# Optimization experiments

Hardware: AMD Instinct MI355X
Metric: run time of the kernel (lower is better)

## Reference

```python
import jax, jax.numpy as jnp
import numpy as np

B, C, N, H = 4, 256, 1024, 8
D = C // H
EPS = 1e-5

def setup_inputs() -> dict:
    key = jax.random.key(0)
    ks = jax.random.split(key, 10)
    s = lambda k, shape: (jax.random.normal(k, shape, jnp.float32) * 0.02)
    return dict(
        node_embeds=jax.random.normal(ks[0], (B, C, N), jnp.float32),
        edge_embeds=jax.random.normal(ks[1], (B, N, N), jnp.float32),
        da_prior=jax.random.normal(ks[2], (B, N, C), jnp.float32),
        gamma=jnp.ones((C,), jnp.float32),
        beta=jnp.zeros((C,), jnp.float32),
        w_qkv=s(ks[3], (C, 3 * C)),            # Linear(node_dim, 3*node_dim), no bias
        w_proj=s(ks[4], (C, C)),
        b_proj=jnp.zeros((C,), jnp.float32),
        w_expand=s(ks[5], (H,)),               # Conv2d(1,H,1) weight (per-head scalar)
        b_expand=jnp.zeros((H,), jnp.float32),
        w_reduce=s(ks[6], (H,)),               # Conv2d(H,1,1) weight
        b_reduce=jnp.zeros((1,), jnp.float32),
        w_fc=s(ks[7], (1, C)),                 # Linear(edge_dim=1, node_dim)
        b_fc=jnp.zeros((C,), jnp.float32),
    )

def reference(node_embeds, edge_embeds, da_prior, gamma, beta, w_qkv,
              w_proj, b_proj, w_expand, b_expand, w_reduce, b_reduce, w_fc, b_fc):
    x = jnp.swapaxes(node_embeds, 1, 2)                       # [B,N,C]
    # einsum 'bnn,bnc->bnc': diagonal of edge matrix scales each node
    diag = jnp.diagonal(edge_embeds, axis1=1, axis2=2)        # [B,N]
    attned = diag[:, :, None] * x                             # [B,N,C]
    # einsum 'bnc,bca->bnc' with prior permuted [B,C,A]: multiply by sum over A
    prior_sum = da_prior.sum(axis=1)                          # [B,C]
    x = attned * prior_sum[:, None, :] + x                    # residual add
    # LayerNorm over channel dim
    mu = x.mean(-1, keepdims=True)
    var = x.var(-1, keepdims=True)
    ln = (x - mu) * jax.lax.rsqrt(var + EPS) * gamma + beta
    qkv = (ln @ w_qkv).reshape(B, N, 3, H, D)
    q = jnp.transpose(qkv[:, :, 0], (0, 2, 1, 3))             # [B,H,N,D]
    k = jnp.transpose(qkv[:, :, 1], (0, 2, 1, 3))
    v = jnp.transpose(qkv[:, :, 2], (0, 2, 1, 3))
    scale = D ** -0.5
    attn = jnp.einsum('bhnd,bhmd->bhnm', q, k) * scale        # [B,H,N,N]
    bias = edge_embeds[:, None] * w_expand[None, :, None, None] + b_expand[None, :, None, None]
    attn = attn + bias                                        # pre-softmax scores = residual
    a = jax.nn.softmax(attn, axis=-1)
    node = jnp.einsum('bhnm,bhmd->bnhd', a, v).reshape(B, N, C)
    # reduce conv over heads on (softmax + residual)
    edge = jnp.einsum('bhnm,h->bnm', a + attn, w_reduce) + b_reduce[0]  # [B,N,N]
    w = jax.nn.softmax(edge, axis=-1)
    wsum = (w * edge).sum(-1)                                 # [B,N]
    node = node + wsum[:, :, None] @ w_fc + b_fc              # fc: [B,N,1]@[1,C]
    node = node @ w_proj + b_proj
    return jnp.swapaxes(node, 1, 2), edge                     # ([B,C,N], [B,N,N])
```

## Files before the change

### kernel.cpp

```cpp
#include <hip/hip_runtime.h>
#include <math.h>

#define Bn 4
#define Cn 256
#define Nn 1024
#define Hn 8
#define Dn 32
#define BHND (Bn * Hn * Nn * Dn)
#define BHN  (Bn * Hn * Nn)

typedef short bf16x8 __attribute__((ext_vector_type(8)));
typedef float f32x4 __attribute__((ext_vector_type(4)));

__device__ inline unsigned f2bf_rn_bits(float x) {
  union { float f; unsigned u; } v; v.f = x;
  return (v.u + 0x7FFFu + ((v.u >> 16) & 1u)) >> 16;
}
__device__ inline float bfbits2f(unsigned b) {
  union { unsigned u; float f; } v; v.u = b << 16; return v.f;
}
__device__ inline void split_bf(float x, unsigned& hi, unsigned& lo) {
  hi = f2bf_rn_bits(x);
  lo = f2bf_rn_bits(x - bfbits2f(hi));
}
__device__ inline unsigned split_bf_trunc_pack(float x) {
  union { float f; unsigned u; } v; v.f = x;
  unsigned hi = v.u >> 16;
  union { unsigned u; float f; } hv; hv.u = hi << 16;
  union { float f; unsigned u; } r; r.f = x - hv.f;
  return hi | (r.u & 0xffff0000u);
}
__device__ inline void unpack_u32x8(const uint4& a, const uint4& b, bf16x8& hi, bf16x8& lo) {
  int4 h4, l4;
  h4.x = (int)((a.x & 0xffffu) | (a.y << 16));  l4.x = (int)((a.x >> 16) | (a.y & 0xffff0000u));
  h4.y = (int)((a.z & 0xffffu) | (a.w << 16));  l4.y = (int)((a.z >> 16) | (a.w & 0xffff0000u));
  h4.z = (int)((b.x & 0xffffu) | (b.y << 16));  l4.z = (int)((b.x >> 16) | (b.y & 0xffff0000u));
  h4.w = (int)((b.z & 0xffffu) | (b.w << 16));  l4.w = (int)((b.z >> 16) | (b.w & 0xffff0000u));
  hi = *(bf16x8*)&h4; lo = *(bf16x8*)&l4;
}

__global__ __launch_bounds__(256) void k_prior_part(const float* __restrict__ dap,
                                                    float* __restrict__ pp) {
  int bi = blockIdx.x;
  int b = bi >> 5, ch = bi & 31;
  int c = threadIdx.x;
  float s = 0.f;
  int n0 = ch * 32;
  for (int n = n0; n < n0 + 32; ++n) s += dap[(size_t)(b * Nn + n) * Cn + c];
  pp[(size_t)(b * 32 + ch) * Cn + c] = s;
}

__global__ __launch_bounds__(256) void k_prior_red(const float* __restrict__ pp,
                                                   float* __restrict__ prior) {
  int i = blockIdx.x * 256 + threadIdx.x;
  int b = i >> 8, c = i & 255;
  float s = 0.f;
  for (int ch = 0; ch < 32; ++ch) s += pp[(size_t)(b * 32 + ch) * Cn + c];
  prior[i] = s;
}

__global__ __launch_bounds__(256) void k_transpose(const float* __restrict__ ne,
                                                   float* __restrict__ xw) {
  __shared__ float tile[32][33];
  int bi = blockIdx.x;
  int b = bi >> 8, rem = bi & 255;
  int c0 = (rem >> 5) << 5;
  int n0 = (rem & 31) << 5;
  int tx = threadIdx.x & 31, ty = threadIdx.x >> 5;
#pragma unroll
  for (int i = 0; i < 4; ++i) {
    int c = c0 + ty + i * 8;
    tile[ty + i * 8][tx] = ne[(size_t)(b * Cn + c) * Nn + n0 + tx];
  }
  __syncthreads();
#pragma unroll
  for (int i = 0; i < 4; ++i) {
    int n = n0 + ty + i * 8;
    xw[(size_t)(b * Nn + n) * Cn + c0 + tx] = tile[tx][ty + i * 8];
  }
}

__global__ __launch_bounds__(256) void k_split_wt(const float* __restrict__ w,
                                                  short* __restrict__ wt_h,
                                                  short* __restrict__ wt_l) {
  __shared__ float tile[32][33];
  int bi = blockIdx.x;
  int j0 = (bi >> 3) << 5;
  int k0 = (bi & 7) << 5;
  int tx = threadIdx.x & 31, ty = threadIdx.x >> 5;
#pragma unroll
  for (int i = 0; i < 4; ++i)
    tile[ty + i * 8][tx] = w[(size_t)(k0 + ty + i * 8) * 768 + j0 + tx];
  __syncthreads();
#pragma unroll
  for (int i = 0; i < 4; ++i) {
    float v = tile[tx][ty + i * 8];
    unsigned hb, lb; split_bf(v, hb, lb);
    wt_h[(size_t)(j0 + ty + i * 8) * 256 + k0 + tx] = (short)hb;
    wt_l[(size_t)(j0 + ty + i * 8) * 256 + k0 + tx] = (short)lb;
  }
}

__global__ __launch_bounds__(256) void k_prep_ln(const float* __restrict__ xw,
                                                 const float* __restrict__ eg,
                                                 const float* __restrict__ prior,
                                                 const float* __restrict__ gamma,
                                                 const float* __restrict__ beta,
                                                 short* __restrict__ ln_h,
                                                 short* __restrict__ ln_l) {
  int bn = blockIdx.x;
  int b = bn >> 10, n = bn & 1023;
  int c = threadIdx.x;
  float x = xw[(size_t)bn * Cn + c];
  float dg = eg[(size_t)(b * Nn + n) * Nn + n];
  float x2 = x * (1.f + dg * prior[b * Cn + c]);
  float s = x2, qq = x2 * x2;
#pragma unroll
  for (int off = 32; off >= 1; off >>= 1) {
    s += __shfl_xor(s, off);
    qq += __shfl_xor(qq, off);
  }
  __shared__ float ss[4], sq[4];
  if ((c & 63) == 0) { ss[c >> 6] = s; sq[c >> 6] = qq; }
  __syncthreads();
  s = ss[0] + ss[1] + ss[2] + ss[3];
  qq = sq[0] + sq[1] + sq[2] + sq[3];
  float mu = s * (1.f / 256.f);
  float var = qq * (1.f / 256.f) - mu * mu;
  float r = rsqrtf(var + 1e-5f);
  float v = (x2 - mu) * r * gamma[c] + beta[c];
  unsigned hb, lb; split_bf(v, hb, lb);
  ln_h[(size_t)bn * Cn + c] = (short)hb;
  ln_l[(size_t)bn * Cn + c] = (short)lb;
}

__global__ __launch_bounds__(256) void k_qkv_mfma(
    const short* __restrict__ ln_h, const short* __restrict__ ln_l,
    const short* __restrict__ wt_h, const short* __restrict__ wt_l,
    short* __restrict__ q_hi, short* __restrict__ q_lo,
    short* __restrict__ k_hi, short* __restrict__ k_lo,
    short* __restrict__ vt_hi, short* __restrict__ vt_lo) {
  __shared__ float ct[64][65];
  int m0 = blockIdx.x * 64;
  int j0 = blockIdx.y * 64;
  int t = threadIdx.x, wid = t >> 6, l = t & 63;
  int lr = l & 15, lq = l >> 4;
  f32x4 acc[4] = {};
  const short* ah_p = ln_h + (size_t)(m0 + wid * 16 + lr) * 256 + lq * 8;
  const short* al_p = ln_l + (size_t)(m0 + wid * 16 + lr) * 256 + lq * 8;
  const short* bh_p = wt_h + (size_t)(j0 + lr) * 256 + lq * 8;
  const short* bl_p = wt_l + (size_t)(j0 + lr) * 256 + lq * 8;
#pragma unroll 2
  for (int k0 = 0; k0 < 256; k0 += 32) {
    bf16x8 ah = *(const bf16x8*)&ah_p[k0];
    bf16x8 al = *(const bf16x8*)&al_p[k0];
#pragma unroll
    for (int js = 0; js < 4; ++js) {
      bf16x8 bh = *(const bf16x8*)&bh_p[js * 16 * 256 + k0];
      bf16x8 bl = *(const bf16x8*)&bl_p[js * 16 * 256 + k0];
      acc[js] = __builtin_amdgcn_mfma_f32_16x16x32_bf16(al, bh, acc[js], 0, 0, 0);
      acc[js] = __builtin_amdgcn_mfma_f32_16x16x32_bf16(ah, bl, acc[js], 0, 0, 0);
      acc[js] = __builtin_amdgcn_mfma_f32_16x16x32_bf16(ah, bh, acc[js], 0, 0, 0);
    }
  }
#pragma unroll
  for (int js = 0; js < 4; ++js)
#pragma unroll
    for (int reg = 0; reg < 4; ++reg)
      ct[wid * 16 + lq * 4 + reg][js * 16 + lr] = acc[js][reg];
  __syncthreads();
  int b = m0 >> 10, n0 = m0 & 1023;
  int three = j0 >> 8;
  const float scale = 0.17677669529663687f;
  if (three == 2) {
    int jl = t >> 2;
    int n4 = (t & 3) * 16;
    int rem = (j0 & 255) + jl;
    int h = rem >> 5, d = rem & 31;
    short hs[16], ls[16];
#pragma unroll
    for (int u = 0; u < 16; ++u) {
      unsigned hb, lb;
      split_bf(ct[n4 + u][jl], hb, lb);
      hs[u] = (short)hb; ls[u] = (short)lb;
    }
    size_t ob = ((size_t)(b * Hn + h) * Dn + d) * Nn + n0 + n4;
    *(uint4*)&vt_hi[ob] = *(uint4*)&hs[0];
    *(uint4*)&vt_hi[ob + 8] = *(uint4*)&hs[8];
    *(uint4*)&vt_lo[ob] = *(uint4*)&ls[0];
    *(uint4*)&vt_lo[ob + 8] = *(uint4*)&ls[8];
  } else {
    int m_l = t & 63, half = t >> 6;
    int rem = (j0 & 255) + half * 16;
    int h = rem >> 5, ddb = rem & 31;
    int n = n0 + m_l;
    float sc = (three == 0) ? 1.0f : scale;
    short* dh = three ? k_hi : q_hi;
    short* dl = three ? k_lo : q_lo;
    short hs[16], ls[16];
#pragma unroll
    for (int u = 0; u < 16; ++u) {
      unsigned hb, lb;
      split_bf(ct[m_l][half * 16 + u] * sc, hb, lb);
      hs[u] = (short)hb; ls[u] = (short)lb;
    }
    size_t base = ((size_t)((b * Hn + h) * Nn + n)) * Dn + ddb;
    *(uint4*)&dh[base] = *(uint4*)&hs[0];
    *(uint4*)&dh[base + 8] = *(uint4*)&hs[8];
    *(uint4*)&dl[base] = *(uint4*)&ls[0];
    *(uint4*)&dl[base + 8] = *(uint4*)&ls[8];
  }
}

__global__ __launch_bounds__(256, 4) void k_attn_core(
    const short* __restrict__ q_hi, const short* __restrict__ q_lo,
    const short* __restrict__ k_hi, const short* __restrict__ k_lo,
    const short* __restrict__ vt_hi, const short* __restrict__ vt_lo,
    const float* __restrict__ eg,
    const float* __restrict__ w_expand, const float* __restrict__ b_expand,
    float* __restrict__ o_part, float* __restrict__ l_part) {
  __shared__ short kh[64 * 40];
  __shared__ short kl[64 * 40];
  __shared__ short vth[32 * 72];
  __shared__ short vtl[32 * 72];
  __shared__ unsigned pbuf[4][16 * 68];

  int blk = blockIdx.x;
  int mh = blk & 1;
  int nt = (blk >> 1) & 15;
  int h = (blk >> 5) & 7;
  int b = blk >> 8;
  int n0 = nt * 64;
  int t = threadIdx.x, wid = t >> 6, l = t & 63;
  int lr = l & 15, lq = l >> 4;

  const float we = w_expand[h], be = b_expand[h];
  size_t bhb = (size_t)(b * Hn + h) * Nn * Dn;
  const short* khg = k_hi + bhb;
  const short* klg = k_lo + bhb;
  const short* vhg = vt_hi + bhb;
  const short* vlg = vt_lo + bhb;

  bf16x8 qhi, qlo;
  {
    size_t qoff = bhb + (size_t)(n0 + wid * 16 + lr) * Dn + lq * 8;
    qhi = *(const bf16x8*)&q_hi[qoff];
    qlo = *(const bf16x8*)&q_lo[qoff];
  }

  f32x4 O0 = {0.f, 0.f, 0.f, 0.f}, O1 = {0.f, 0.f, 0.f, 0.f};
  float rowsum[4] = {0.f, 0.f, 0.f, 0.f};
  int nrow = n0 + wid * 16 + lq * 4;

  for (int ms = 0; ms < 8; ++ms) {
    int m0 = mh * 512 + ms * 64;
    float eb[4][4];
#pragma unroll
    for (int reg = 0; reg < 4; ++reg) {
      const float* ep = &eg[(size_t)(b * Nn + nrow + reg) * Nn + m0 + lr];
#pragma unroll
      for (int msub = 0; msub < 4; ++msub) eb[msub][reg] = ep[msub * 16];
    }
    __syncthreads();
    {
      int row = t >> 2, c = (t & 3) * 8;
      *(uint4*)&kh[row * 40 + c] = *(const uint4*)&khg[(size_t)(m0 + row) * Dn + c];
      *(uint4*)&kl[row * 40 + c] = *(const uint4*)&klg[(size_t)(m0 + row) * Dn + c];
      int d = t >> 3, cm = (t & 7) * 8;
      *(uint4*)&vth[d * 72 + cm] = *(const uint4*)&vhg[(size_t)d * Nn + m0 + cm];
      *(uint4*)&vtl[d * 72 + cm] = *(const uint4*)&vlg[(size_t)d * Nn + m0 + cm];
    }
    __syncthreads();

#pragma unroll
    for (int msub = 0; msub < 4; ++msub) {
      int mrow = msub * 16 + lr;
      bf16x8 bh8 = *(bf16x8*)&kh[mrow * 40 + lq * 8];
      bf16x8 bl8 = *(bf16x8*)&kl[mrow * 40 + lq * 8];
      f32x4 sacc = {0.f, 0.f, 0.f, 0.f};
      sacc = __builtin_amdgcn_mfma_f32_16x16x32_bf16(qlo, bh8, sacc, 0, 0, 0);
      sacc = __builtin_amdgcn_mfma_f32_16x16x32_bf16(qhi, bl8, sacc, 0, 0, 0);
      sacc = __builtin_amdgcn_mfma_f32_16x16x32_bf16(qhi, bh8, sacc, 0, 0, 0);
#pragma unroll
      for (int reg = 0; reg < 4; ++reg) {
        float s = sacc[reg] + eb[msub][reg] * we + be;
        float e = __expf(s);
        rowsum[reg] += e;
        pbuf[wid][(lq * 4 + reg) * 68 + msub * 16 + lr] = split_bf_trunc_pack(e);
      }
    }

#pragma unroll
    for (int mw = 0; mw < 2; ++mw) {
      uint4 pa = *(uint4*)&pbuf[wid][lr * 68 + mw * 32 + lq * 8];
      uint4 pb = *(uint4*)&pbuf[wid][lr * 68 + mw * 32 + lq * 8 + 4];
      bf16x8 ahi, alo;
      unpack_u32x8(pa, pb, ahi, alo);
      {
        bf16x8 vh8 = *(bf16x8*)&vth[lr * 72 + mw * 32 + lq * 8];
        bf16x8 vl8 = *(bf16x8*)&vtl[lr * 72 + mw * 32 + lq * 8];
        O0 = __builtin_amdgcn_mfma_f32_16x16x32_bf16(alo, vh8, O0, 0, 0, 0);
        O0 = __builtin_amdgcn_mfma_f32_16x16x32_bf16(ahi, vl8, O0, 0, 0, 0);
        O0 = __builtin_amdgcn_mfma_f32_16x16x32_bf16(ahi, vh8, O0, 0, 0, 0);
      }
      {
        bf16x8 vh8 = *(bf16x8*)&vth[(16 + lr) * 72 + mw * 32 + lq * 8];
        bf16x8 vl8 = *(bf16x8*)&vtl[(16 + lr) * 72 + mw * 32 + lq * 8];
        O1 = __builtin_amdgcn_mfma_f32_16x16x32_bf16(alo, vh8, O1, 0, 0, 0);
        O1 = __builtin_amdgcn_mfma_f32_16x16x32_bf16(ahi, vl8, O1, 0, 0, 0);
        O1 = __builtin_amdgcn_mfma_f32_16x16x32_bf16(ahi, vh8, O1, 0, 0, 0);
      }
    }
  }

#pragma unroll
  for (int reg = 0; reg < 4; ++reg) {
#pragma unroll
    for (int off = 1; off < 16; off <<= 1)
      rowsum[reg] += __shfl_xor(rowsum[reg], off);
  }
  size_t pbase = (size_t)mh * BHND + bhb;
#pragma unroll
  for (int reg = 0; reg < 4; ++reg) {
    int n = nrow + reg;
    o_part[pbase + (size_t)n * Dn + lr] = O0[reg];
    o_part[pbase + (size_t)n * Dn + 16 + lr] = O1[reg];
    if (lr == 0)
      l_part[(size_t)mh * BHN + (size_t)(b * Hn + h) * Nn + n] = rowsum[reg];
  }
}

__global__ __launch_bounds__(256, 4) void k_edge_mfma(
    const short* __restrict__ q_hi, const short* __restrict__ q_lo,
    const short* __restrict__ k_hi, const short* __restrict__ k_lo,
    const float* __restrict__ eg, const float* __restrict__ l_part,
    const float* __restrict__ w_expand, const float* __restrict__ b_expand,
    const float* __restrict__ w_reduce, const float* __restrict__ b_reduce,
    float* __restrict__ edge_out, float* __restrict__ pl_part,
    float* __restrict__ pwe_part) {
  __shared__ short kh[64 * 40];
  __shared__ short kl[64 * 40];
  int blk = blockIdx.x;
  int mt = blk & 15;
  int nt = (blk >> 4) & 15;
  int b = blk >> 8;
  int n0 = nt * 64, m0 = mt * 64;
  int t = threadIdx.x, wid = t >> 6, l = t & 63;
  int lr = l & 15, lq = l >> 4;
  const float br = b_reduce[0];
  int nrow = n0 + wid * 16 + lq * 4;

  float eacc[4][4], ebias[4][4];
#pragma unroll
  for (int reg = 0; reg < 4; ++reg) {
    const float* ep = &eg[(size_t)(b * Nn + nrow + reg) * Nn + m0 + lr];
#pragma unroll
    for (int msub = 0; msub < 4; ++msub) {
      ebias[msub][reg] = ep[msub * 16];
      eacc[msub][reg] = br;
    }
  }

  for (int h = 0; h < Hn; ++h) {
    size_t bhb = (size_t)(b * Hn + h) * Nn * Dn;
    float we = w_expand[h], be = b_expand[h], wr = w_reduce[h];
    bf16x8 qhi, qlo;
    {
      size_t qoff = bhb + (size_t)(n0 + wid * 16 + lr) * Dn + lq * 8;
      qhi = *(const bf16x8*)&q_hi[qoff];
      qlo = *(const bf16x8*)&q_lo[qoff];
    }
    float invl[4];
#pragma unroll
    for (int reg = 0; reg < 4; ++reg) {
      size_t idx = (size_t)(b * Hn + h) * Nn + nrow + reg;
      invl[reg] = 1.0f / (l_part[idx] + l_part[BHN + idx]);
    }

    __syncthreads();
    {
      int row = t >> 2, c = (t & 3) * 8;
      *(uint4*)&kh[row * 40 + c] = *(const uint4*)&k_hi[bhb + (size_t)(m0 + row) * Dn + c];
      *(uint4*)&kl[row * 40 + c] = *(const uint4*)&k_lo[bhb + (size_t)(m0 + row) * Dn + c];
    }
    __syncthreads();
#pragma unroll
    for (int msub = 0; msub < 4; ++msub) {
      int mrow = msub * 16 + lr;
      bf16x8 bh8 = *(bf16x8*)&kh[mrow * 40 + lq * 8];
      bf16x8 bl8 = *(bf16x8*)&kl[mrow * 40 + lq * 8];
      f32x4 sacc = {0.f, 0.f, 0.f, 0.f};
      sacc = __builtin_amdgcn_mfma_f32_16x16x32_bf16(qlo, bh8, sacc, 0, 0, 0);
      sacc = __builtin_amdgcn_mfma_f32_16x16x32_bf16(qhi, bl8, sacc, 0, 0, 0);
      sacc = __builtin_amdgcn_mfma_f32_16x16x32_bf16(qhi, bh8, sacc, 0, 0, 0);
#pragma unroll
      for (int reg = 0; reg < 4; ++reg) {
        float s = sacc[reg] + ebias[msub][reg] * we + be;
        float p = __expf(s) * invl[reg];
        eacc[msub][reg] += wr * (p + s);
      }
    }
  }
#pragma unroll
  for (int msub = 0; msub < 4; ++msub)
#pragma unroll
    for (int reg = 0; reg < 4; ++reg)
      edge_out[(size_t)(b * Nn + nrow + reg) * Nn + m0 + msub * 16 + lr] = eacc[msub][reg];

  float pl[4] = {0.f, 0.f, 0.f, 0.f}, pw[4] = {0.f, 0.f, 0.f, 0.f};
#pragma unroll
  for (int msub = 0; msub < 4; ++msub)
#pragma unroll
    for (int reg = 0; reg < 4; ++reg) {
      float e = eacc[msub][reg];
      float x = __expf(e);
      pl[reg] += x;
      pw[reg] += x * e;
    }
#pragma unroll
  for (int reg = 0; reg < 4; ++reg) {
#pragma unroll
    for (int off = 1; off < 16; off <<= 1) {
      pl[reg] += __shfl_xor(pl[reg], off);
      pw[reg] += __shfl_xor(pw[reg], off);
    }
    if (lr == 0) {
      int idx = mt * (Bn * Nn) + b * Nn + nrow + reg;
      pl_part[idx] = pl[reg];
      pwe_part[idx] = pw[reg];
    }
  }
}

__global__ __launch_bounds__(256) void k_edge_red(const float* __restrict__ pl,
                                                  const float* __restrict__ pwe,
                                                  float* __restrict__ wsum) {
  int i = blockIdx.x * 256 + threadIdx.x;
  float L = 0.f, Wv = 0.f;
  for (int mt = 0; mt < 16; ++mt) {
    L += pl[mt * (Bn * Nn) + i];
    Wv += pwe[mt * (Bn * Nn) + i];
  }
  wsum[i] = Wv / L;
}

__global__ __launch_bounds__(256) void k_proj_gemm(const float* __restrict__ o_part,
                                                   const float* __restrict__ l_part,
                                                   const float* __restrict__ wsum,
                                                   const float* __restrict__ wfc,
                                                   const float* __restrict__ bfc,
                                                   const float* __restrict__ wproj,
                                                   const float* __restrict__ bproj,
                                                   float* __restrict__ out) {
  __shared__ __align__(16) float at[16][68];
  __shared__ __align__(16) float bt[16][68];
  __shared__ float ct[64][65];
  int m0 = blockIdx.x * 64;
  int j0 = blockIdx.y * 64;
  int t = threadIdx.x;
  int tx = t & 15, ty = t >> 4;
  float4 acc[4] = {};
  for (int k0 = 0; k0 < 256; k0 += 16) {
    {
      int row = t >> 2, k4 = (t & 3) << 2;
      int m = m0 + row;
      int bb = m >> 10, n = m & 1023;
      int c = k0 + k4;
      int h = c >> 5, dd = c & 31;
      float wsm = wsum[m];
      size_t ob = ((size_t)(bb * Hn + h) * Nn + n) * Dn + dd;
      float4 oa = *(const float4*)&o_part[ob];
      float4 oc = *(const float4*)&o_part[BHND + ob];
      size_t sidx = (size_t)(bb * Hn + h) * Nn + n;
      float inv = 1.0f / (l_part[sidx] + l_part[BHN + sidx]);
      float4 a;
      a.x = (oa.x + oc.x) * inv + wsm * wfc[c + 0] + bfc[c + 0];
      a.y = (oa.y + oc.y) * inv + wsm * wfc[c + 1] + bfc[c + 1];
      a.z = (oa.z + oc.z) * inv + wsm * wfc[c + 2] + bfc[c + 2];
      a.w = (oa.w + oc.w) * inv + wsm * wfc[c + 3] + bfc[c + 3];
      at[k4 + 0][row] = a.x; at[k4 + 1][row] = a.y;
      at[k4 + 2][row] = a.z; at[k4 + 3][row] = a.w;
      int rb = t >> 4, jb = (t & 15) << 2;
      *(float4*)&bt[rb][jb] = *(const float4*)&wproj[(size_t)(k0 + rb) * 256 + j0 + jb];
    }
    __syncthreads();
#pragma unroll
    for (int kk = 0; kk < 16; ++kk) {
      float4 a4 = *(float4*)&at[kk][ty << 2];
      float4 b4 = *(float4*)&bt[kk][tx << 2];
      acc[0].x += a4.x * b4.x; acc[0].y += a4.x * b4.y; acc[0].z += a4.x * b4.z; acc[0].w += a4.x * b4.w;
      acc[1].x += a4.y * b4.x; acc[1].y += a4.y * b4.y; acc[1].z += a4.y * b4.z; acc[1].w += a4.y * b4.w;
      acc[2].x += a4.z * b4.x; acc[2].y += a4.z * b4.y; acc[2].z += a4.z * b4.z; acc[2].w += a4.z * b4.w;
      acc[3].x += a4.w * b4.x; acc[3].y += a4.w * b4.y; acc[3].z += a4.w * b4.z; acc[3].w += a4.w * b4.w;
    }
    __syncthreads();
  }
#pragma unroll
  for (int i = 0; i < 4; ++i) {
    ct[(ty << 2) + i][(tx << 2) + 0] = acc[i].x + bproj[j0 + (tx << 2) + 0];
    ct[(ty << 2) + i][(tx << 2) + 1] = acc[i].y + bproj[j0 + (tx << 2) + 1];
    ct[(ty << 2) + i][(tx << 2) + 2] = acc[i].z + bproj[j0 + (tx << 2) + 2];
    ct[(ty << 2) + i][(tx << 2) + 3] = acc[i].w + bproj[j0 + (tx << 2) + 3];
  }
  __syncthreads();
  int b = m0 >> 10, n0 = m0 & 1023;
  int n4 = t & 15, c0i = t >> 4;
#pragma unroll
  for (int u = 0; u < 4; ++u) {
    int ci = c0i + u * 16;
    float4 val = { ct[(n4 << 2) + 0][ci], ct[(n4 << 2) + 1][ci],
                   ct[(n4 << 2) + 2][ci], ct[(n4 << 2) + 3][ci] };
    *(float4*)&out[(size_t)(b * Cn + j0 + ci) * Nn + n0 + (n4 << 2)] = val;
  }
}

extern "C" void kernel_launch(void* const* d_in, const int* in_sizes, int n_in,
                              void* d_out, int out_size, void* d_ws, size_t ws_size,
                              hipStream_t stream) {
  (void)in_sizes; (void)n_in; (void)out_size; (void)ws_size;
  const float* node_embeds = (const float*)d_in[0];
  const float* edge_embeds = (const float*)d_in[1];
  const float* da_prior    = (const float*)d_in[2];
  const float* gamma       = (const float*)d_in[3];
  const float* beta        = (const float*)d_in[4];
  const float* w_qkv       = (const float*)d_in[5];
  const float* w_proj      = (const float*)d_in[6];
  const float* b_proj      = (const float*)d_in[7];
  const float* w_expand    = (const float*)d_in[8];
  const float* b_expand    = (const float*)d_in[9];
  const float* w_reduce    = (const float*)d_in[10];
  const float* b_reduce    = (const float*)d_in[11];
  const float* w_fc        = (const float*)d_in[12];
  const float* b_fc        = (const float*)d_in[13];
  float* out_node = (float*)d_out;
  float* out_edge = out_node + (size_t)Bn * Cn * Nn;

  const size_t M = 1048576;
  float* W = (float*)d_ws;
  float* ws_x   = W;
  short* ln_hi  = (short*)(W + M);
  short* ln_lo  = ln_hi + M;
  float* o_part = W;
  short* vt_hi  = (short*)(W + 2 * M);
  short* vt_lo  = vt_hi + M;
  short* q_hi   = (short*)(W + 3 * M);
  short* q_lo   = q_hi + M;
  short* k_hi   = q_hi + 2 * M;
  short* k_lo   = q_hi + 3 * M;
  float* ws_pp    = W + 5 * M;
  float* ws_prior = ws_pp + Bn * 32 * Cn;
  float* ws_wsum  = ws_prior + Bn * Cn;
  float* l_part   = ws_wsum + Bn * Nn;
  float* pl_part  = l_part + 2 * BHN;
  float* pwe_part = pl_part + 16 * Bn * Nn;
  short* wt_hi    = (short*)(pwe_part + 16 * Bn * Nn);
  short* wt_lo    = wt_hi + 768 * 256;

  k_split_wt<<<dim3(192), dim3(256), 0, stream>>>(w_qkv, wt_hi, wt_lo);
  k_prior_part<<<dim3(Bn * 32), dim3(256), 0, stream>>>(da_prior, ws_pp);
  k_prior_red<<<dim3(Bn), dim3(256), 0, stream>>>(ws_pp, ws_prior);
  k_transpose<<<dim3(Bn * 256), dim3(256), 0, stream>>>(node_embeds, ws_x);
  k_prep_ln<<<dim3(Bn * Nn), dim3(256), 0, stream>>>(ws_x, edge_embeds, ws_prior,
                                                     gamma, beta, ln_hi, ln_lo);
  k_qkv_mfma<<<dim3(64, 12), dim3(256), 0, stream>>>(ln_hi, ln_lo, wt_hi, wt_lo,
                                                     q_hi, q_lo, k_hi, k_lo,
                                                     vt_hi, vt_lo);
  k_attn_core<<<dim3(Bn * Hn * 16 * 2), dim3(256), 0, stream>>>(
      q_hi, q_lo, k_hi, k_lo, vt_hi, vt_lo, edge_embeds, w_expand, b_expand,
      o_part, l_part);
  k_edge_mfma<<<dim3(Bn * 16 * 16), dim3(256), 0, stream>>>(
      q_hi, q_lo, k_hi, k_lo, edge_embeds, l_part, w_expand, b_expand,
      w_reduce, b_reduce, out_edge, pl_part, pwe_part);
  k_edge_red<<<dim3(16), dim3(256), 0, stream>>>(pl_part, pwe_part, ws_wsum);
  k_proj_gemm<<<dim3(64, 4), dim3(256), 0, stream>>>(o_part, l_part, ws_wsum,
                                                     w_fc, b_fc, w_proj, b_proj,
                                                     out_node);
}
```

Before: 206.2 us.

## Fuse small preprocessing and reduction kernels to cut launch count

Merges the prior partial sum and the weight split/transpose into one kernel. The transpose kernel is dropped: the LayerNorm prep now reads node_embeds directly with a strided column access and finishes the prior reduction inline. The edge-softmax reduction moves into the projection GEMM prologue. This cuts four launches and several workspace round trips. In exchange, the LayerNorm kernel's global reads become uncoalesced and the projection blocks repeat a small reduction.

```diff
diff --git a/kernel.cpp b/kernel.cpp
--- a/kernel.cpp
+++ b/kernel.cpp
@@ -39,71 +39,42 @@
   hi = *(bf16x8*)&h4; lo = *(bf16x8*)&l4;
 }
 
-__global__ __launch_bounds__(256) void k_prior_part(const float* __restrict__ dap,
-                                                    float* __restrict__ pp) {
-  int bi = blockIdx.x;
-  int b = bi >> 5, ch = bi & 31;
-  int c = threadIdx.x;
-  float s = 0.f;
-  int n0 = ch * 32;
-  for (int n = n0; n < n0 + 32; ++n) s += dap[(size_t)(b * Nn + n) * Cn + c];
-  pp[(size_t)(b * 32 + ch) * Cn + c] = s;
-}
-
-__global__ __launch_bounds__(256) void k_prior_red(const float* __restrict__ pp,
-                                                   float* __restrict__ prior) {
-  int i = blockIdx.x * 256 + threadIdx.x;
-  int b = i >> 8, c = i & 255;
-  float s = 0.f;
-  for (int ch = 0; ch < 32; ++ch) s += pp[(size_t)(b * 32 + ch) * Cn + c];
-  prior[i] = s;
-}
-
-__global__ __launch_bounds__(256) void k_transpose(const float* __restrict__ ne,
-                                                   float* __restrict__ xw) {
+__global__ __launch_bounds__(256) void k_pre(const float* __restrict__ w,
+                                             const float* __restrict__ dap,
+                                             short* __restrict__ wt_h,
+                                             short* __restrict__ wt_l,
+                                             float* __restrict__ pp) {
   __shared__ float tile[32][33];
   int bi = blockIdx.x;
-  int b = bi >> 8, rem = bi & 255;
-  int c0 = (rem >> 5) << 5;
-  int n0 = (rem & 31) << 5;
-  int tx = threadIdx.x & 31, ty = threadIdx.x >> 5;
-#pragma unroll
-  for (int i = 0; i < 4; ++i) {
-    int c = c0 + ty + i * 8;
-    tile[ty + i * 8][tx] = ne[(size_t)(b * Cn + c) * Nn + n0 + tx];
-  }
-  __syncthreads();
-#pragma unroll
-  for (int i = 0; i < 4; ++i) {
-    int n = n0 + ty + i * 8;
-    xw[(size_t)(b * Nn + n) * Cn + c0 + tx] = tile[tx][ty + i * 8];
-  }
-}
-
-__global__ __launch_bounds__(256) void k_split_wt(const float* __restrict__ w,
-                                                  short* __restrict__ wt_h,
-                                                  short* __restrict__ wt_l) {
-  __shared__ float tile[32][33];
-  int bi = blockIdx.x;
-  int j0 = (bi >> 3) << 5;
-  int k0 = (bi & 7) << 5;
-  int tx = threadIdx.x & 31, ty = threadIdx.x >> 5;
-#pragma unroll
-  for (int i = 0; i < 4; ++i)
-    tile[ty + i * 8][tx] = w[(size_t)(k0 + ty + i * 8) * 768 + j0 + tx];
-  __syncthreads();
-#pragma unroll
-  for (int i = 0; i < 4; ++i) {
-    float v = tile[tx][ty + i * 8];
-    unsigned hb, lb; split_bf(v, hb, lb);
-    wt_h[(size_t)(j0 + ty + i * 8) * 256 + k0 + tx] = (short)hb;
-    wt_l[(size_t)(j0 + ty + i * 8) * 256 + k0 + tx] = (short)lb;
-  }
-}
-
-__global__ __launch_bounds__(256) void k_prep_ln(const float* __restrict__ xw,
+  if (bi < 32) {
+    int b = bi >> 3, ch = bi & 7;
+    int c = threadIdx.x;
+    float s = 0.f;
+    int n0 = ch * 128;
+    for (int n = n0; n < n0 + 128; ++n) s += dap[(size_t)(b * Nn + n) * Cn + c];
+    pp[(size_t)bi * Cn + c] = s;
+  } else {
+    int wi = bi - 32;
+    int j0 = (wi >> 3) << 5;
+    int k0 = (wi & 7) << 5;
+    int tx = threadIdx.x & 31, ty = threadIdx.x >> 5;
+#pragma unroll
+    for (int i = 0; i < 4; ++i)
+      tile[ty + i * 8][tx] = w[(size_t)(k0 + ty + i * 8) * 768 + j0 + tx];
+    __syncthreads();
+#pragma unroll
+    for (int i = 0; i < 4; ++i) {
+      float v = tile[tx][ty + i * 8];
+      unsigned hb, lb; split_bf(v, hb, lb);
+      wt_h[(size_t)(j0 + ty + i * 8) * 256 + k0 + tx] = (short)hb;
+      wt_l[(size_t)(j0 + ty + i * 8) * 256 + k0 + tx] = (short)lb;
+    }
+  }
+}
+
+__global__ __launch_bounds__(256) void k_prep_ln(const float* __restrict__ ne,
                                                  const float* __restrict__ eg,
-                                                 const float* __restrict__ prior,
+                                                 const float* __restrict__ pp,
                                                  const float* __restrict__ gamma,
                                                  const float* __restrict__ beta,
                                                  short* __restrict__ ln_h,
@@ -111,9 +82,12 @@
   int bn = blockIdx.x;
   int b = bn >> 10, n = bn & 1023;
   int c = threadIdx.x;
-  float x = xw[(size_t)bn * Cn + c];
+  float x = ne[(size_t)(b * Cn + c) * Nn + n];
+  float pr = 0.f;
+#pragma unroll
+  for (int ch = 0; ch < 8; ++ch) pr += pp[(size_t)(b * 8 + ch) * Cn + c];
   float dg = eg[(size_t)(b * Nn + n) * Nn + n];
-  float x2 = x * (1.f + dg * prior[b * Cn + c]);
+  float x2 = x * (1.f + dg * pr);
   float s = x2, qq = x2 * x2;
 #pragma unroll
   for (int off = 32; off >= 1; off >>= 1) {
@@ -432,21 +406,10 @@
   }
 }
 
-__global__ __launch_bounds__(256) void k_edge_red(const float* __restrict__ pl,
-                                                  const float* __restrict__ pwe,
-                                                  float* __restrict__ wsum) {
-  int i = blockIdx.x * 256 + threadIdx.x;
-  float L = 0.f, Wv = 0.f;
-  for (int mt = 0; mt < 16; ++mt) {
-    L += pl[mt * (Bn * Nn) + i];
-    Wv += pwe[mt * (Bn * Nn) + i];
-  }
-  wsum[i] = Wv / L;
-}
-
 __global__ __launch_bounds__(256) void k_proj_gemm(const float* __restrict__ o_part,
                                                    const float* __restrict__ l_part,
-                                                   const float* __restrict__ wsum,
+                                                   const float* __restrict__ pl,
+                                                   const float* __restrict__ pwe,
                                                    const float* __restrict__ wfc,
                                                    const float* __restrict__ bfc,
                                                    const float* __restrict__ wproj,
@@ -455,10 +418,22 @@
   __shared__ __align__(16) float at[16][68];
   __shared__ __align__(16) float bt[16][68];
   __shared__ float ct[64][65];
+  __shared__ float wsm_s[64];
   int m0 = blockIdx.x * 64;
   int j0 = blockIdx.y * 64;
   int t = threadIdx.x;
   int tx = t & 15, ty = t >> 4;
+  if (t < 64) {
+    int m = m0 + t;
+    float L = 0.f, Wv = 0.f;
+#pragma unroll
+    for (int mt = 0; mt < 16; ++mt) {
+      L += pl[mt * (Bn * Nn) + m];
+      Wv += pwe[mt * (Bn * Nn) + m];
+    }
+    wsm_s[t] = Wv / L;
+  }
+  __syncthreads();
   float4 acc[4] = {};
   for (int k0 = 0; k0 < 256; k0 += 16) {
     {
@@ -467,7 +442,7 @@
       int bb = m >> 10, n = m & 1023;
       int c = k0 + k4;
       int h = c >> 5, dd = c & 31;
-      float wsm = wsum[m];
+      float wsm = wsm_s[row];
       size_t ob = ((size_t)(bb * Hn + h) * Nn + n) * Dn + dd;
       float4 oa = *(const float4*)&o_part[ob];
       float4 oc = *(const float4*)&o_part[BHND + ob];
@@ -537,7 +512,6 @@
 
   const size_t M = 1048576;
   float* W = (float*)d_ws;
-  float* ws_x   = W;
   short* ln_hi  = (short*)(W + M);
   short* ln_lo  = ln_hi + M;
   float* o_part = W;
@@ -548,19 +522,14 @@
   short* k_hi   = q_hi + 2 * M;
   short* k_lo   = q_hi + 3 * M;
   float* ws_pp    = W + 5 * M;
-  float* ws_prior = ws_pp + Bn * 32 * Cn;
-  float* ws_wsum  = ws_prior + Bn * Cn;
-  float* l_part   = ws_wsum + Bn * Nn;
+  float* l_part   = ws_pp + Bn * 8 * Cn;
   float* pl_part  = l_part + 2 * BHN;
   float* pwe_part = pl_part + 16 * Bn * Nn;
   short* wt_hi    = (short*)(pwe_part + 16 * Bn * Nn);
   short* wt_lo    = wt_hi + 768 * 256;
 
-  k_split_wt<<<dim3(192), dim3(256), 0, stream>>>(w_qkv, wt_hi, wt_lo);
-  k_prior_part<<<dim3(Bn * 32), dim3(256), 0, stream>>>(da_prior, ws_pp);
-  k_prior_red<<<dim3(Bn), dim3(256), 0, stream>>>(ws_pp, ws_prior);
-  k_transpose<<<dim3(Bn * 256), dim3(256), 0, stream>>>(node_embeds, ws_x);
-  k_prep_ln<<<dim3(Bn * Nn), dim3(256), 0, stream>>>(ws_x, edge_embeds, ws_prior,
+  k_pre<<<dim3(224), dim3(256), 0, stream>>>(w_qkv, da_prior, wt_hi, wt_lo, ws_pp);
+  k_prep_ln<<<dim3(Bn * Nn), dim3(256), 0, stream>>>(node_embeds, edge_embeds, ws_pp,
                                                      gamma, beta, ln_hi, ln_lo);
   k_qkv_mfma<<<dim3(64, 12), dim3(256), 0, stream>>>(ln_hi, ln_lo, wt_hi, wt_lo,
                                                      q_hi, q_lo, k_hi, k_lo,
@@ -571,8 +540,7 @@
   k_edge_mfma<<<dim3(Bn * 16 * 16), dim3(256), 0, stream>>>(
       q_hi, q_lo, k_hi, k_lo, edge_embeds, l_part, w_expand, b_expand,
       w_reduce, b_reduce, out_edge, pl_part, pwe_part);
-  k_edge_red<<<dim3(16), dim3(256), 0, stream>>>(pl_part, pwe_part, ws_wsum);
-  k_proj_gemm<<<dim3(64, 4), dim3(256), 0, stream>>>(o_part, l_part, ws_wsum,
-                                                     w_fc, b_fc, w_proj, b_proj,
-                                                     out_node);
-}
+  k_proj_gemm<<<dim3(64, 4), dim3(256), 0, stream>>>(o_part, l_part, pl_part,
+                                                     pwe_part, w_fc, b_fc,
+                                                     w_proj, b_proj, out_node);
+}
```

Result: no change. 202.2 us (-1.9%).
